# Performance work log

Hardware: AMD Instinct MI355X
Metric: run time of the kernel (lower is better)

Reference implementation:

```python
import jax, jax.numpy as jnp
import numpy as np

H = 32  # hidden size


def _lstm_layer(x_sbi, w_ih, w_hh, b_ih, b_hh):
    # x_sbi: [S, B, in]; w_ih: [4H, in]; w_hh: [4H, H] (torch gate order i,f,g,o)
    S, B, _ = x_sbi.shape
    # precompute input projections for all timesteps: [S, B, 4H]
    xg = jnp.einsum('sbi,gi->sbg', x_sbi, w_ih) + (b_ih + b_hh)

    def step(carry, xg_t):
        h, c = carry
        gates = xg_t + h @ w_hh.T  # [B, 4H]
        i, f, g, o = jnp.split(gates, 4, axis=-1)
        i = jax.nn.sigmoid(i)
        f = jax.nn.sigmoid(f)
        g = jnp.tanh(g)
        o = jax.nn.sigmoid(o)
        c = f * c + i * g
        h = o * jnp.tanh(c)
        return (h, c), h

    h0 = jnp.zeros((B, H), x_sbi.dtype)
    c0 = jnp.zeros((B, H), x_sbi.dtype)
    (h_last, _), hs = jax.lax.scan(step, (h0, c0), xg)
    return hs, h_last  # hs: [S, B, H]


def setup_inputs() -> dict:
    key = jax.random.key(0)
    ks = jax.random.split(key, 12)
    B, S = 4096, 512
    s = 1.0 / np.sqrt(H)  # torch default uniform(-1/sqrt(H), 1/sqrt(H))
    u = lambda k, shape: jax.random.uniform(k, shape, jnp.float32, -s, s)
    return {
        'x': jax.random.normal(ks[0], (B, S, 1), jnp.float32),
        'w_ih0': u(ks[1], (4 * H, 1)),
        'w_hh0': u(ks[2], (4 * H, H)),
        'b_ih0': u(ks[3], (4 * H,)),
        'b_hh0': u(ks[4], (4 * H,)),
        'w_ih1': u(ks[5], (4 * H, H)),
        'w_hh1': u(ks[6], (4 * H, H)),
        'b_ih1': u(ks[7], (4 * H,)),
        'b_hh1': u(ks[8], (4 * H,)),
        'fc1_w': u(ks[9], (16, H)),
        'fc1_b': u(ks[9], (16,)),
        'fc2_w': u(ks[10], (1, 16)),
        'fc2_b': u(ks[11], (1,)),
    }


def reference(x, w_ih0, w_hh0, b_ih0, b_hh0, w_ih1, w_hh1, b_ih1, b_hh1,
              fc1_w, fc1_b, fc2_w, fc2_b):
    x_sbi = jnp.swapaxes(x, 0, 1)  # [S, B, 1]
    hs1, _ = _lstm_layer(x_sbi, w_ih0, w_hh0, b_ih0, b_hh0)
    _, h_last = _lstm_layer(hs1, w_ih1, w_hh1, b_ih1, b_hh1)  # last timestep of layer 2
    y = h_last @ fc1_w.T + fc1_b
    y = jnp.where(y >= 0, y, 0.2 * y)  # leaky_relu(0.2)
    y = y @ fc2_w.T + fc2_b
    return y  # [B, 1]
```

## Files before the change

### kernel.cpp

```cpp
#include <hip/hip_runtime.h>

#define H 32
#define SEQ 512
#define BM 16
#define NTHREADS 1024
#define HSTRIDE 40

typedef _Float16 half8 __attribute__((ext_vector_type(8)));
typedef __attribute__((ext_vector_type(4))) float f32x4;

#define L2E 1.44269504088896340736f

__device__ __forceinline__ float rcp_(float x)  { return __builtin_amdgcn_rcpf(x); }
__device__ __forceinline__ float exp2_(float x) { return __builtin_amdgcn_exp2f(x); }
#define MFMA16(A, B, C) __builtin_amdgcn_mfma_f32_16x16x32_f16((A), (B), (C), 0, 0, 0)

__device__ __forceinline__ float cell(const f32x4& g, float& cst) {
    float ei = exp2_(g[0]), ef = exp2_(g[1]), eg = exp2_(g[2]), eo = exp2_(g[3]);
    float A  = 1.f + ei, F = 1.f + ef;
    float Gp = eg + 1.f, Gm = eg - 1.f;
    float t1 = A * Gp;
    float num = fmaf(cst, t1, Gm * F);
    float cn  = num * rcp_(F * t1);
    cst = cn;
    float ec = exp2_(fminf(cn * (2.f * L2E), 80.f));
    return (ec - 1.f) * rcp_((1.f + eo) * (ec + 1.f));
}

__global__ __launch_bounds__(NTHREADS, 4) void lstm_kernel(
    const float* __restrict__ x,
    const float* __restrict__ w_ih0,
    const float* __restrict__ w_hh0,
    const float* __restrict__ b_ih0, const float* __restrict__ b_hh0,
    const float* __restrict__ w_ih1,
    const float* __restrict__ w_hh1,
    const float* __restrict__ b_ih1, const float* __restrict__ b_hh1,
    const float* __restrict__ fc1_w,
    const float* __restrict__ fc1_b,
    const float* __restrict__ fc2_w,
    const float* __restrict__ fc2_b,
    float* __restrict__ out)
{
    __shared__ __align__(16) float    xbufT[SEQ * BM];
    __shared__ __align__(16) _Float16 h1s[4][BM * HSTRIDE];
    __shared__ __align__(16) _Float16 h2s[2][BM * HSTRIDE];
    __shared__ __align__(16) float    h2f[BM * 33];
    __shared__ __align__(16) float    yb[BM * 17];

    const int tid  = threadIdx.x;
    const int lane = tid & 63;
    const int wv   = tid >> 6;
    const int role = wv >> 3;
    const int w    = wv & 7;
    const int c    = lane & 15;
    const int q    = lane >> 4;
    const int r0   = blockIdx.x * BM;

    {
        const int row = tid >> 6;
        const int s0  = (tid & 63) * 8;
        const float* xr = x + (size_t)(r0 + row) * SEQ + s0;
        #pragma unroll
        for (int i = 0; i < 8; i += 4) {
            float4 v = *(const float4*)&xr[i];
            xbufT[(s0 + i + 0) * BM + row] = v.x;
            xbufT[(s0 + i + 1) * BM + row] = v.y;
            xbufT[(s0 + i + 2) * BM + row] = v.z;
            xbufT[(s0 + i + 3) * BM + row] = v.w;
        }
    }
    for (int i = tid; i < 4 * BM * HSTRIDE; i += NTHREADS) ((_Float16*)h1s)[i] = (_Float16)0.f;
    for (int i = tid; i < 2 * BM * HSTRIDE; i += NTHREADS) ((_Float16*)h2s)[i] = (_Float16)0.f;

    const float gsc[4] = { -L2E, -L2E, 2.f * L2E, -L2E };
    const int worig = (c & 3) * H + 4 * w + (c >> 2);
    const float wsc = gsc[c & 3];
    const int kb = 8 * q;
    const int m = c;
    const int u = 4 * w + q;

    half8 wa = {}, wb = {};
    f32x4 biasv;
    float wx0 = 0.f, wx1 = 0.f, wx2 = 0.f, wx3 = 0.f;
    if (role == 0) {
        const float* p = &w_hh0[worig * H + kb];
        #pragma unroll
        for (int j = 0; j < 8; ++j) wa[j] = (_Float16)(p[j] * wsc);
        #pragma unroll
        for (int g = 0; g < 4; ++g) biasv[g] = (b_ih0[g * H + u] + b_hh0[g * H + u]) * gsc[g];
        wx0 = w_ih0[0 * H + u] * gsc[0];
        wx1 = w_ih0[1 * H + u] * gsc[1];
        wx2 = w_ih0[2 * H + u] * gsc[2];
        wx3 = w_ih0[3 * H + u] * gsc[3];
    } else {
        const float* p = &w_ih1[worig * H + kb];
        #pragma unroll
        for (int j = 0; j < 8; ++j) wa[j] = (_Float16)(p[j] * wsc);
        p = &w_hh1[worig * H + kb];
        #pragma unroll
        for (int j = 0; j < 8; ++j) wb[j] = (_Float16)(p[j] * wsc);
        #pragma unroll
        for (int g = 0; g < 4; ++g) biasv[g] = (b_ih1[g * H + u] + b_hh1[g * H + u]) * gsc[g];
    }

    float cst = 0.f;
    float hlast = 0.f;

    const int fofs  = c * HSTRIDE + kb;
    const int whofs = m * HSTRIDE + u;

    __syncthreads();

    for (int tb = 0; tb < 516; tb += 4) {
        #pragma unroll
        for (int p = 0; p < 4; ++p) {
            const int t = tb + p;
            if (role == 0) {
                if (t < 512) {
                    half8 a1 = *(const half8*)(&h1s[(p + 3) & 3][0] + fofs);
                    float xv = xbufT[t * BM + m];
                    f32x4 g1 = MFMA16(wa, a1, biasv);
                    g1[0] = fmaf(xv, wx0, g1[0]);
                    g1[1] = fmaf(xv, wx1, g1[1]);
                    g1[2] = fmaf(xv, wx2, g1[2]);
                    g1[3] = fmaf(xv, wx3, g1[3]);
                    float hv = cell(g1, cst);
                    h1s[p][whofs] = (_Float16)hv;
                }
            } else {
                if (t >= 2 && t < 514) {
                    half8 a1L = *(const half8*)(&h1s[(p + 2) & 3][0] + fofs);
                    half8 a2  = *(const half8*)(&h2s[(p + 1) & 1][0] + fofs);
                    f32x4 g2 = MFMA16(wb, a2, MFMA16(wa, a1L, biasv));
                    float hv = cell(g2, cst);
                    hlast = hv;
                    h2s[p & 1][whofs] = (_Float16)hv;
                }
            }
            __syncthreads();
        }
    }

    if (role == 1) h2f[m * 33 + u] = hlast;
    __syncthreads();
    if (tid < BM * 16) {
        int rr = tid >> 4, j = tid & 15;
        float acc = fc1_b[j];
        #pragma unroll
        for (int k = 0; k < H; ++k) acc += fc1_w[j * H + k] * h2f[rr * 33 + k];
        acc = acc >= 0.f ? acc : 0.2f * acc;
        yb[rr * 17 + j] = acc * fc2_w[j];
    }
    __syncthreads();
    if (tid < BM) {
        float acc = fc2_b[0];
        #pragma unroll
        for (int j = 0; j < 16; ++j) acc += yb[tid * 17 + j];
        out[r0 + tid] = acc;
    }
}

extern "C" void kernel_launch(void* const* d_in, const int* in_sizes, int n_in,
                              void* d_out, int out_size, void* d_ws, size_t ws_size,
                              hipStream_t stream) {
    const float* x     = (const float*)d_in[0];
    const float* w_ih0 = (const float*)d_in[1];
    const float* w_hh0 = (const float*)d_in[2];
    const float* b_ih0 = (const float*)d_in[3];
    const float* b_hh0 = (const float*)d_in[4];
    const float* w_ih1 = (const float*)d_in[5];
    const float* w_hh1 = (const float*)d_in[6];
    const float* b_ih1 = (const float*)d_in[7];
    const float* b_hh1 = (const float*)d_in[8];
    const float* fc1_w = (const float*)d_in[9];
    const float* fc1_b = (const float*)d_in[10];
    const float* fc2_w = (const float*)d_in[11];
    const float* fc2_b = (const float*)d_in[12];
    float* out = (float*)d_out;

    const int B = in_sizes[0] / SEQ;
    hipLaunchKernelGGL(lstm_kernel, dim3(B / BM), dim3(NTHREADS), 0, stream,
                       x, w_ih0, w_hh0, b_ih0, b_hh0, w_ih1, w_hh1, b_ih1, b_hh1,
                       fc1_w, fc1_b, fc2_w, fc2_b, out);
}
```

Baseline: 274.6 us.

## Shrink block to 4 waves, each computing four hidden-unit tiles per step

Cuts the block from 16 waves to 4 waves (2 per layer). Each wave now handles four 16x16 MFMA gate tiles per timestep instead of one, and the input projection is folded into the MFMA accumulator. The aim is cheaper per-step __syncthreads barriers and more instruction-level parallelism within each wave. In exchange, each wave has a longer serial chain of MFMA and transcendental work per step, and register pressure rises.

Result: slower. 322.7 us (+17.5%).

```diff
diff --git a/kernel.cpp b/kernel.cpp
--- a/kernel.cpp
+++ b/kernel.cpp
@@ -3,7 +3,7 @@
 #define H 32
 #define SEQ 512
 #define BM 16
-#define NTHREADS 1024
+#define NTHREADS 256
 #define HSTRIDE 40
 
 typedef _Float16 half8 __attribute__((ext_vector_type(8)));
@@ -27,7 +27,7 @@
     return (ec - 1.f) * rcp_((1.f + eo) * (ec + 1.f));
 }
 
-__global__ __launch_bounds__(NTHREADS, 4) void lstm_kernel(
+__global__ __launch_bounds__(NTHREADS, 1) void lstm_kernel(
     const float* __restrict__ x,
     const float* __restrict__ w_ih0,
     const float* __restrict__ w_hh0,
@@ -50,18 +50,18 @@
     const int tid  = threadIdx.x;
     const int lane = tid & 63;
     const int wv   = tid >> 6;
-    const int role = wv >> 3;
-    const int w    = wv & 7;
+    const int role = wv >> 1;
+    const int uh   = wv & 1;
     const int c    = lane & 15;
     const int q    = lane >> 4;
     const int r0   = blockIdx.x * BM;
 
     {
-        const int row = tid >> 6;
-        const int s0  = (tid & 63) * 8;
+        const int row = tid >> 4;
+        const int s0  = (tid & 15) * 32;
         const float* xr = x + (size_t)(r0 + row) * SEQ + s0;
         #pragma unroll
-        for (int i = 0; i < 8; i += 4) {
+        for (int i = 0; i < 32; i += 4) {
             float4 v = *(const float4*)&xr[i];
             xbufT[(s0 + i + 0) * BM + row] = v.x;
             xbufT[(s0 + i + 1) * BM + row] = v.y;
@@ -73,41 +73,45 @@
     for (int i = tid; i < 2 * BM * HSTRIDE; i += NTHREADS) ((_Float16*)h2s)[i] = (_Float16)0.f;
 
     const float gsc[4] = { -L2E, -L2E, 2.f * L2E, -L2E };
-    const int worig = (c & 3) * H + 4 * w + (c >> 2);
     const float wsc = gsc[c & 3];
     const int kb = 8 * q;
     const int m = c;
-    const int u = 4 * w + q;
-
-    half8 wa = {}, wb = {};
-    f32x4 biasv;
-    float wx0 = 0.f, wx1 = 0.f, wx2 = 0.f, wx3 = 0.f;
-    if (role == 0) {
-        const float* p = &w_hh0[worig * H + kb];
-        #pragma unroll
-        for (int j = 0; j < 8; ++j) wa[j] = (_Float16)(p[j] * wsc);
-        #pragma unroll
-        for (int g = 0; g < 4; ++g) biasv[g] = (b_ih0[g * H + u] + b_hh0[g * H + u]) * gsc[g];
-        wx0 = w_ih0[0 * H + u] * gsc[0];
-        wx1 = w_ih0[1 * H + u] * gsc[1];
-        wx2 = w_ih0[2 * H + u] * gsc[2];
-        wx3 = w_ih0[3 * H + u] * gsc[3];
-    } else {
-        const float* p = &w_ih1[worig * H + kb];
-        #pragma unroll
-        for (int j = 0; j < 8; ++j) wa[j] = (_Float16)(p[j] * wsc);
-        p = &w_hh1[worig * H + kb];
-        #pragma unroll
-        for (int j = 0; j < 8; ++j) wb[j] = (_Float16)(p[j] * wsc);
-        #pragma unroll
-        for (int g = 0; g < 4; ++g) biasv[g] = (b_ih1[g * H + u] + b_hh1[g * H + u]) * gsc[g];
-    }
-
-    float cst = 0.f;
-    float hlast = 0.f;
-
-    const int fofs  = c * HSTRIDE + kb;
-    const int whofs = m * HSTRIDE + u;
+
+    half8 wA[4], wB[4];
+    f32x4 biasv[4], wxv[4];
+    int   wof[4];
+    #pragma unroll
+    for (int k = 0; k < 4; ++k) {
+        const int u0    = 16 * uh + 4 * k;
+        const int u     = u0 + q;
+        const int worig = (c & 3) * H + u0 + (c >> 2);
+        wof[k] = m * HSTRIDE + u;
+        if (role == 0) {
+            const float* p = &w_hh0[worig * H + kb];
+            #pragma unroll
+            for (int j = 0; j < 8; ++j) wA[k][j] = (_Float16)(p[j] * wsc);
+            #pragma unroll
+            for (int g = 0; g < 4; ++g) {
+                biasv[k][g] = (b_ih0[g * H + u] + b_hh0[g * H + u]) * gsc[g];
+                wxv[k][g]   = w_ih0[g * H + u] * gsc[g];
+            }
+        } else {
+            const float* p = &w_ih1[worig * H + kb];
+            #pragma unroll
+            for (int j = 0; j < 8; ++j) wA[k][j] = (_Float16)(p[j] * wsc);
+            p = &w_hh1[worig * H + kb];
+            #pragma unroll
+            for (int j = 0; j < 8; ++j) wB[k][j] = (_Float16)(p[j] * wsc);
+            #pragma unroll
+            for (int g = 0; g < 4; ++g)
+                biasv[k][g] = (b_ih1[g * H + u] + b_hh1[g * H + u]) * gsc[g];
+        }
+    }
+
+    float cst[4] = {0.f, 0.f, 0.f, 0.f};
+    float hl[4]  = {0.f, 0.f, 0.f, 0.f};
+
+    const int fofs = c * HSTRIDE + kb;
 
     __syncthreads();
 
@@ -117,33 +121,48 @@
             const int t = tb + p;
             if (role == 0) {
                 if (t < 512) {
+                    float xv = xbufT[t * BM + m];
+                    f32x4 pre[4];
+                    #pragma unroll
+                    for (int k = 0; k < 4; ++k) {
+                        #pragma unroll
+                        for (int j = 0; j < 4; ++j) pre[k][j] = fmaf(xv, wxv[k][j], biasv[k][j]);
+                    }
                     half8 a1 = *(const half8*)(&h1s[(p + 3) & 3][0] + fofs);
-                    float xv = xbufT[t * BM + m];
-                    f32x4 g1 = MFMA16(wa, a1, biasv);
-                    g1[0] = fmaf(xv, wx0, g1[0]);
-                    g1[1] = fmaf(xv, wx1, g1[1]);
-                    g1[2] = fmaf(xv, wx2, g1[2]);
-                    g1[3] = fmaf(xv, wx3, g1[3]);
-                    float hv = cell(g1, cst);
-                    h1s[p][whofs] = (_Float16)hv;
+                    f32x4 g1[4];
+                    #pragma unroll
+                    for (int k = 0; k < 4; ++k) g1[k] = MFMA16(wA[k], a1, pre[k]);
+                    #pragma unroll
+                    for (int k = 0; k < 4; ++k) {
+                        float hv = cell(g1[k], cst[k]);
+                        h1s[p][wof[k]] = (_Float16)hv;
+                    }
                 }
             } else {
                 if (t >= 2 && t < 514) {
                     half8 a1L = *(const half8*)(&h1s[(p + 2) & 3][0] + fofs);
                     half8 a2  = *(const half8*)(&h2s[(p + 1) & 1][0] + fofs);
-                    f32x4 g2 = MFMA16(wb, a2, MFMA16(wa, a1L, biasv));
-                    float hv = cell(g2, cst);
-                    hlast = hv;
-                    h2s[p & 1][whofs] = (_Float16)hv;
+                    f32x4 g2[4];
+                    #pragma unroll
+                    for (int k = 0; k < 4; ++k) g2[k] = MFMA16(wB[k], a2, MFMA16(wA[k], a1L, biasv[k]));
+                    #pragma unroll
+                    for (int k = 0; k < 4; ++k) {
+                        float hv = cell(g2[k], cst[k]);
+                        hl[k] = hv;
+                        h2s[p & 1][wof[k]] = (_Float16)hv;
+                    }
                 }
             }
             __syncthreads();
         }
     }
 
-    if (role == 1) h2f[m * 33 + u] = hlast;
+    if (role == 1) {
+        #pragma unroll
+        for (int k = 0; k < 4; ++k) h2f[m * 33 + (16 * uh + 4 * k + q)] = hl[k];
+    }
     __syncthreads();
-    if (tid < BM * 16) {
+    {
         int rr = tid >> 4, j = tid & 15;
         float acc = fc1_b[j];
         #pragma unroll
```
